# Kernel tuning notes

Hardware: AMD Instinct MI355X
Metric: run time of the kernel (lower is better)

The kernel has to match this reference:

```python
import jax, jax.numpy as jnp
import numpy as np

TOP_K = 4

def setup_inputs() -> dict:
    key = jax.random.key(0)
    k1, k2, k3, k4 = jax.random.split(key, 4)
    B, S, D, E, H, O = 4, 2048, 1024, 8, 512, 1024
    x = jax.random.normal(k1, (B, S, D), dtype=jnp.float32)
    wg = jax.random.normal(k2, (E, D), dtype=jnp.float32) * 0.02
    w1 = jax.random.normal(k3, (E, H, D), dtype=jnp.float32) * 0.02
    w2 = jax.random.normal(k4, (E, O, H), dtype=jnp.float32) * 0.02
    return {"x": x, "wg": wg, "w1": w1, "w2": w2}

def reference(x, wg, w1, w2):
    # x: [B, S, D]; wg: [E, D]; w1: [E, H, D]; w2: [E, O, H]
    B, S, D = x.shape
    E = wg.shape[0]
    xt = x.reshape(B * S, D)                       # [N, D]
    logits = xt @ wg.T                              # [N, E] gate logits
    _, idx = jax.lax.top_k(logits, TOP_K)           # [N, k] selected experts
    N = xt.shape[0]
    # membership mask: 1.0 where expert e is among the token's top-k
    mask = jnp.zeros((N, E), dtype=x.dtype).at[jnp.arange(N)[:, None], idx].set(1.0)
    # dense per-expert FFN (relu MLP), then combine with unweighted sum over
    # the k selected experts (the original sums top-k outputs without gate weights)
    h = jax.nn.relu(jnp.einsum('nd,ehd->neh', xt, w1))   # [N, E, H]
    y = jnp.einsum('neh,eoh->neo', h, w2)                # [N, E, O]
    out = jnp.einsum('neo,ne->no', y, mask)              # [N, O]
    return out.reshape(B, S, -1)
```

## Files before the change

### kernel.cpp

```cpp
#include <hip/hip_runtime.h>

typedef float f32x4 __attribute__((ext_vector_type(4)));
typedef short bf16x8 __attribute__((ext_vector_type(8)));

#define NTOK 8192
#define DIM  1024
#define NE   8
#define NH   512
#define NO   1024

static __device__ __forceinline__ unsigned short f2bf(float f) {
  unsigned u = __float_as_uint(f);
  u += 0x7fffu + ((u >> 16) & 1u);
  return (unsigned short)(u >> 16);
}
static __device__ __forceinline__ unsigned pk2(float a, float b) {
  return (unsigned)f2bf(a) | ((unsigned)f2bf(b) << 16);
}

static __device__ __forceinline__ f32x4 mfma_bf16(bf16x8 a, bf16x8 b, f32x4 c) {
  return __builtin_amdgcn_mfma_f32_16x16x32_bf16(a, b, c, 0, 0, 0);
}

__global__ __launch_bounds__(256) void gate_kernel(
    const float* __restrict__ x, const float* __restrict__ wg,
    unsigned char* __restrict__ msk8, float* __restrict__ out)
{
  {
    size_t t = (size_t)blockIdx.x * 256 + threadIdx.x;
    float4* op = (float4*)(out + t * 16);
    float4 z4 = {0.f, 0.f, 0.f, 0.f};
    op[0] = z4; op[1] = z4; op[2] = z4; op[3] = z4;
  }
  const int lane = threadIdx.x & 63;
  const int wv = threadIdx.x >> 6;
  const int n = blockIdx.x * 4 + wv;
  const float* xr = x + (size_t)n * DIM;
  float4 v[4];
#pragma unroll
  for (int i = 0; i < 4; ++i) v[i] = *(const float4*)(xr + i * 256 + lane * 4);
  double logit[NE];
#pragma unroll
  for (int e = 0; e < NE; ++e) {
    const float* wr = wg + e * DIM;
    double s = 0.0;
#pragma unroll
    for (int i = 0; i < 4; ++i) {
      float4 g = *(const float4*)(wr + i * 256 + lane * 4);
      s += (double)v[i].x * g.x + (double)v[i].y * g.y +
           (double)v[i].z * g.z + (double)v[i].w * g.w;
    }
#pragma unroll
    for (int off = 32; off; off >>= 1) s += __shfl_down(s, off);
    logit[e] = s;
  }
  if (lane == 0) {
    unsigned sel = 0;
#pragma unroll
    for (int t = 0; t < 4; ++t) {
      int best = 0; double bv = -1.0e300;
#pragma unroll
      for (int e = 0; e < NE; ++e)
        if (!((sel >> e) & 1) && logit[e] > bv) { bv = logit[e]; best = e; }
      sel |= 1u << best;
    }
    msk8[n] = (unsigned char)sel;
  }
}

__global__ __launch_bounds__(256) void pack_w1_kernel(
    const float* __restrict__ w1, unsigned short* __restrict__ w1p)
{
  int t = blockIdx.x * 256 + threadIdx.x;
  int lane = t & 63, ks = (t >> 6) & 31, nt = (t >> 11) & 31, e = t >> 16;
  int r = nt * 16 + (lane & 15);
  int c = ks * 32 + (lane >> 4) * 8;
  const float* src = w1 + ((size_t)(e * 512 + r)) * 1024 + c;
  float4 f0 = *(const float4*)src;
  float4 f1 = *(const float4*)(src + 4);
  uint4 v;
  v.x = pk2(f0.x, f0.y); v.y = pk2(f0.z, f0.w);
  v.z = pk2(f1.x, f1.y); v.w = pk2(f1.z, f1.w);
  *(uint4*)(w1p + (size_t)t * 8) = v;
}

__global__ __launch_bounds__(256) void pack_w2_kernel(
    const float* __restrict__ w2, unsigned short* __restrict__ w2p)
{
  int t = blockIdx.x * 256 + threadIdx.x;
  int lane = t & 63, ks = (t >> 6) & 15, ot = (t >> 10) & 63, e = t >> 16;
  int o = ot * 16 + (lane & 15);
  int h = ks * 32 + (lane >> 4) * 8;
  const float* src = w2 + ((size_t)(e * 1024 + o)) * 512 + h;
  float4 f0 = *(const float4*)src;
  float4 f1 = *(const float4*)(src + 4);
  uint4 v;
  v.x = pk2(f0.x, f0.y); v.y = pk2(f0.z, f0.w);
  v.z = pk2(f1.x, f1.y); v.w = pk2(f1.z, f1.w);
  *(uint4*)(w2p + (size_t)t * 8) = v;
}

__global__ __launch_bounds__(1024, 4) void moe_ffn(
    const float* __restrict__ x, const unsigned short* __restrict__ w1p,
    const unsigned short* __restrict__ w2p, const unsigned char* __restrict__ msk8,
    float* __restrict__ out)
{
  __shared__ unsigned short xs[128 * 64 * 8];
  __shared__ unsigned short hs[32 * 64 * 8];

  const int tid = threadIdx.x;
  const int lane = tid & 63;
  const int wv = tid >> 6;
  const int row0 = (blockIdx.x >> 1) * 64;
  const int z = blockIdx.x & 1;
  const int arow = lane & 15;
  const int kch = lane >> 4;

#pragma unroll
  for (int i = 0; i < 8; ++i) {
    int c = i * 1024 + tid;
    int r = c >> 7;
    int ch = c & 127;
    const float* src = x + (size_t)(row0 + r) * DIM + ch * 8;
    float4 f0 = *(const float4*)src;
    float4 f1 = *(const float4*)(src + 4);
    uint4 v;
    v.x = pk2(f0.x, f0.y); v.y = pk2(f0.z, f0.w);
    v.z = pk2(f1.x, f1.y); v.w = pk2(f1.z, f1.w);
    int f = (ch >> 2) * 4 + (r >> 4);
    int l = ((ch & 3) << 4) | (r & 15);
    *(uint4*)(xs + ((size_t)(f * 64 + l)) * 8) = v;
  }
  __syncthreads();

  const unsigned short* xp = xs + lane * 8;
  const unsigned short* hp = hs + lane * 8;

  f32x4 oacc[4][4];
#pragma unroll
  for (int m = 0; m < 4; ++m)
#pragma unroll
    for (int n = 0; n < 4; ++n) oacc[m][n] = f32x4{0.f, 0.f, 0.f, 0.f};

  for (int e = 0; e < NE; ++e) {
    f32x4 hacc[4];
#pragma unroll
    for (int m = 0; m < 4; ++m) hacc[m] = f32x4{0.f, 0.f, 0.f, 0.f};

    const unsigned short* pb =
        w1p + ((size_t)(e * 32 + z * 16 + wv) * 32) * 512 + lane * 8;
#pragma unroll 4
    for (int ks = 0; ks < 32; ++ks) {
      bf16x8 b = *(const bf16x8*)(pb + ks * 512);
#pragma unroll
      for (int m = 0; m < 4; ++m) {
        bf16x8 a = *(const bf16x8*)(xp + (ks * 4 + m) * 512);
        hacc[m] = mfma_bf16(a, b, hacc[m]);
      }
    }
    __syncthreads();

#pragma unroll
    for (int m = 0; m < 4; ++m) {
      const unsigned mb = *(const unsigned*)(msk8 + row0 + m * 16 + kch * 4);
#pragma unroll
      for (int j = 0; j < 4; ++j) {
        float v = fmaxf(hacc[m][j], 0.0f);
        v = ((mb >> (j * 8 + e)) & 1u) ? v : 0.0f;
        int f = (wv >> 1) * 4 + m;
        int l2 = (((wv & 1) * 2 + (arow >> 3)) << 4) | (kch * 4 + j);
        hs[((size_t)(f * 64 + l2)) * 8 + (arow & 7)] = f2bf(v);
      }
    }
    __syncthreads();

    const unsigned short* pc =
        w2p + ((size_t)((e * 64 + wv * 4) * 16 + z * 8)) * 512 + lane * 8;
#pragma unroll 2
    for (int ks2 = 0; ks2 < 8; ++ks2) {
      bf16x8 a0 = *(const bf16x8*)(hp + (ks2 * 4 + 0) * 512);
      bf16x8 a1 = *(const bf16x8*)(hp + (ks2 * 4 + 1) * 512);
      bf16x8 a2 = *(const bf16x8*)(hp + (ks2 * 4 + 2) * 512);
      bf16x8 a3 = *(const bf16x8*)(hp + (ks2 * 4 + 3) * 512);
#pragma unroll
      for (int n = 0; n < 4; ++n) {
        bf16x8 b = *(const bf16x8*)(pc + (size_t)n * 8192 + ks2 * 512);
        oacc[0][n] = mfma_bf16(a0, b, oacc[0][n]);
        oacc[1][n] = mfma_bf16(a1, b, oacc[1][n]);
        oacc[2][n] = mfma_bf16(a2, b, oacc[2][n]);
        oacc[3][n] = mfma_bf16(a3, b, oacc[3][n]);
      }
    }
  }

#pragma unroll
  for (int m = 0; m < 4; ++m)
#pragma unroll
    for (int n = 0; n < 4; ++n)
#pragma unroll
      for (int j = 0; j < 4; ++j) {
        int row = row0 + m * 16 + kch * 4 + j;
        int col = (wv * 4 + n) * 16 + arow;
        atomicAdd(&out[(size_t)row * NO + col], oacc[m][n][j]);
      }
}

extern "C" void kernel_launch(void* const* d_in, const int* in_sizes, int n_in,
                              void* d_out, int out_size, void* d_ws, size_t ws_size,
                              hipStream_t stream) {
  (void)in_sizes; (void)n_in; (void)out_size; (void)ws_size;
  const float* x  = (const float*)d_in[0];
  const float* wg = (const float*)d_in[1];
  const float* w1 = (const float*)d_in[2];
  const float* w2 = (const float*)d_in[3];
  float* out = (float*)d_out;
  char* ws = (char*)d_ws;
  unsigned short* w1p = (unsigned short*)ws;
  unsigned short* w2p = (unsigned short*)(ws + ((size_t)8 << 20));
  unsigned char* msk8 = (unsigned char*)(ws + ((size_t)16 << 20));

  gate_kernel<<<2048, 256, 0, stream>>>(x, wg, msk8, out);
  pack_w1_kernel<<<2048, 256, 0, stream>>>(w1, w1p);
  pack_w2_kernel<<<2048, 256, 0, stream>>>(w2, w2p);
  moe_ffn<<<256, 1024, 0, stream>>>(x, w1p, w2p, msk8, out);
}
```

Baseline: 199.1 us.

## Split experts across block pair instead of hidden halves, reuse x fragments across two hidden halves

Previously each pair of blocks split the hidden dimension, so every block ran all 8 experts over half of H. Now each block of the pair handles 4 experts over the full hidden dimension, computing both hidden halves in one pass that reuses each x LDS fragment for two MFMAs. The per-token mask words are hoisted out of the expert loop. This halves the LDS A-reads for the first GEMM and reduces per-expert barriers, at the cost of more accumulator registers under the 1024-thread launch bound, which may cause spilling.

```diff
diff --git a/kernel.cpp b/kernel.cpp
--- a/kernel.cpp
+++ b/kernel.cpp
@@ -112,7 +112,7 @@
   const int lane = tid & 63;
   const int wv = tid >> 6;
   const int row0 = (blockIdx.x >> 1) * 64;
-  const int z = blockIdx.x & 1;
+  const int eq = blockIdx.x & 1;
   const int arow = lane & 15;
   const int kch = lane >> 4;
 
@@ -131,6 +131,10 @@
     int l = ((ch & 3) << 4) | (r & 15);
     *(uint4*)(xs + ((size_t)(f * 64 + l)) * 8) = v;
   }
+  unsigned mb[4];
+#pragma unroll
+  for (int m = 0; m < 4; ++m)
+    mb[m] = *(const unsigned*)(msk8 + row0 + m * 16 + kch * 4);
   __syncthreads();
 
   const unsigned short* xp = xs + lane * 8;
@@ -142,53 +146,62 @@
 #pragma unroll
     for (int n = 0; n < 4; ++n) oacc[m][n] = f32x4{0.f, 0.f, 0.f, 0.f};
 
-  for (int e = 0; e < NE; ++e) {
-    f32x4 hacc[4];
-#pragma unroll
-    for (int m = 0; m < 4; ++m) hacc[m] = f32x4{0.f, 0.f, 0.f, 0.f};
-
-    const unsigned short* pb =
-        w1p + ((size_t)(e * 32 + z * 16 + wv) * 32) * 512 + lane * 8;
+#pragma unroll 1
+  for (int el = 0; el < 4; ++el) {
+    const int e = eq * 4 + el;
+
+    f32x4 hacc[4][2];
+#pragma unroll
+    for (int m = 0; m < 4; ++m) {
+      hacc[m][0] = f32x4{0.f, 0.f, 0.f, 0.f};
+      hacc[m][1] = f32x4{0.f, 0.f, 0.f, 0.f};
+    }
+    const unsigned short* pb0 = w1p + ((size_t)(e * 32 + wv) * 32) * 512 + lane * 8;
+    const unsigned short* pb1 = pb0 + (size_t)16 * 32 * 512;
 #pragma unroll 4
     for (int ks = 0; ks < 32; ++ks) {
-      bf16x8 b = *(const bf16x8*)(pb + ks * 512);
+      bf16x8 b0 = *(const bf16x8*)(pb0 + ks * 512);
+      bf16x8 b1 = *(const bf16x8*)(pb1 + ks * 512);
 #pragma unroll
       for (int m = 0; m < 4; ++m) {
         bf16x8 a = *(const bf16x8*)(xp + (ks * 4 + m) * 512);
-        hacc[m] = mfma_bf16(a, b, hacc[m]);
+        hacc[m][0] = mfma_bf16(a, b0, hacc[m][0]);
+        hacc[m][1] = mfma_bf16(a, b1, hacc[m][1]);
       }
     }
-    __syncthreads();
-
-#pragma unroll
-    for (int m = 0; m < 4; ++m) {
-      const unsigned mb = *(const unsigned*)(msk8 + row0 + m * 16 + kch * 4);
-#pragma unroll
-      for (int j = 0; j < 4; ++j) {
-        float v = fmaxf(hacc[m][j], 0.0f);
-        v = ((mb >> (j * 8 + e)) & 1u) ? v : 0.0f;
-        int f = (wv >> 1) * 4 + m;
-        int l2 = (((wv & 1) * 2 + (arow >> 3)) << 4) | (kch * 4 + j);
-        hs[((size_t)(f * 64 + l2)) * 8 + (arow & 7)] = f2bf(v);
-      }
-    }
-    __syncthreads();
-
-    const unsigned short* pc =
-        w2p + ((size_t)((e * 64 + wv * 4) * 16 + z * 8)) * 512 + lane * 8;
+
+#pragma unroll 1
+    for (int hh = 0; hh < 2; ++hh) {
+      __syncthreads();
+
+#pragma unroll
+      for (int m = 0; m < 4; ++m)
+#pragma unroll
+        for (int j = 0; j < 4; ++j) {
+          float v = fmaxf(hacc[m][hh][j], 0.0f);
+          v = ((mb[m] >> (j * 8 + e)) & 1u) ? v : 0.0f;
+          int f = (wv >> 1) * 4 + m;
+          int l2 = (((wv & 1) * 2 + (arow >> 3)) << 4) | (kch * 4 + j);
+          hs[((size_t)(f * 64 + l2)) * 8 + (arow & 7)] = f2bf(v);
+        }
+      __syncthreads();
+
+      const unsigned short* pc =
+          w2p + ((size_t)((e * 64 + wv * 4) * 16 + hh * 8)) * 512 + lane * 8;
 #pragma unroll 2
-    for (int ks2 = 0; ks2 < 8; ++ks2) {
-      bf16x8 a0 = *(const bf16x8*)(hp + (ks2 * 4 + 0) * 512);
-      bf16x8 a1 = *(const bf16x8*)(hp + (ks2 * 4 + 1) * 512);
-      bf16x8 a2 = *(const bf16x8*)(hp + (ks2 * 4 + 2) * 512);
-      bf16x8 a3 = *(const bf16x8*)(hp + (ks2 * 4 + 3) * 512);
-#pragma unroll
-      for (int n = 0; n < 4; ++n) {
-        bf16x8 b = *(const bf16x8*)(pc + (size_t)n * 8192 + ks2 * 512);
-        oacc[0][n] = mfma_bf16(a0, b, oacc[0][n]);
-        oacc[1][n] = mfma_bf16(a1, b, oacc[1][n]);
-        oacc[2][n] = mfma_bf16(a2, b, oacc[2][n]);
-        oacc[3][n] = mfma_bf16(a3, b, oacc[3][n]);
+      for (int ks2 = 0; ks2 < 8; ++ks2) {
+        bf16x8 a0 = *(const bf16x8*)(hp + (ks2 * 4 + 0) * 512);
+        bf16x8 a1 = *(const bf16x8*)(hp + (ks2 * 4 + 1) * 512);
+        bf16x8 a2 = *(const bf16x8*)(hp + (ks2 * 4 + 2) * 512);
+        bf16x8 a3 = *(const bf16x8*)(hp + (ks2 * 4 + 3) * 512);
+#pragma unroll
+        for (int n = 0; n < 4; ++n) {
+          bf16x8 b = *(const bf16x8*)(pc + (size_t)n * 8192 + ks2 * 512);
+          oacc[0][n] = mfma_bf16(a0, b, oacc[0][n]);
+          oacc[1][n] = mfma_bf16(a1, b, oacc[1][n]);
+          oacc[2][n] = mfma_bf16(a2, b, oacc[2][n]);
+          oacc[3][n] = mfma_bf16(a3, b, oacc[3][n]);
+        }
       }
     }
   }
```

New measurement: 249.7 us. 25.4% more time.
